# Performance work log

Measured on AMD Instinct MI355X. Metric: run time of the kernel, lower is better.

## Reference

```python
import jax, jax.numpy as jnp
import numpy as np

B, S, D, H = 2, 2048, 1024, 16
DH = D // H
DFF = 4 * D
EPS = 1e-5


def layernorm(x, g, b):
    mu = jnp.mean(x, axis=-1, keepdims=True)
    var = jnp.mean(jnp.square(x - mu), axis=-1, keepdims=True)
    return (x - mu) * jax.lax.rsqrt(var + EPS) * g + b


def setup_inputs() -> dict:
    key = jax.random.key(0)
    ks = jax.random.split(key, 12)
    s = 0.02
    return {
        "x": jax.random.normal(ks[0], (B, S, D), dtype=jnp.float32),
        "ln1_g": jnp.ones((D,), jnp.float32),
        "ln1_b": jnp.zeros((D,), jnp.float32),
        "Wq": jax.random.normal(ks[1], (D, D), jnp.float32) * s,
        "bq": jnp.zeros((D,), jnp.float32),
        "Wk": jax.random.normal(ks[2], (D, D), jnp.float32) * s,
        "bk": jnp.zeros((D,), jnp.float32),
        "Wv": jax.random.normal(ks[3], (D, D), jnp.float32) * s,
        "bv": jnp.zeros((D,), jnp.float32),
        "Wo": jax.random.normal(ks[4], (D, D), jnp.float32) * s,
        "bo": jnp.zeros((D,), jnp.float32),
        "ln2_g": jnp.ones((D,), jnp.float32),
        "ln2_b": jnp.zeros((D,), jnp.float32),
        "W1": jax.random.normal(ks[5], (D, DFF), jnp.float32) * s,
        "b1": jnp.zeros((DFF,), jnp.float32),
        "W2": jax.random.normal(ks[6], (DFF, D), jnp.float32) * s,
        "b2": jnp.zeros((D,), jnp.float32),
    }


def block(x, ln1_g, ln1_b, Wq, bq, Wk, bk, Wv, bv, Wo, bo, ln2_g, ln2_b, W1, b1, W2, b2):
    h = layernorm(x, ln1_g, ln1_b)
    # projections -> [B, H, S, DH]
    q = (h @ Wq + bq).reshape(B, S, H, DH).transpose(0, 2, 1, 3)
    k = (h @ Wk + bk).reshape(B, S, H, DH).transpose(0, 2, 1, 3)
    v = (h @ Wv + bv).reshape(B, S, H, DH).transpose(0, 2, 1, 3)
    scores = jnp.einsum('bhqd,bhkd->bhqk', q, k) / jnp.sqrt(jnp.float32(DH))
    causal = jnp.tril(jnp.ones((S, S), dtype=bool))  # True = keep
    scores = jnp.where(causal, scores, -jnp.inf)
    attn = jax.nn.softmax(scores, axis=-1)
    out = jnp.einsum('bhqk,bhkd->bhqd', attn, v)
    out = out.transpose(0, 2, 1, 3).reshape(B, S, D)
    x = x + out @ Wo + bo
    h2 = layernorm(x, ln2_g, ln2_b)
    ff = jax.nn.gelu(h2 @ W1 + b1, approximate=False) @ W2 + b2
    return x + ff


def reference(x, ln1_g, ln1_b, Wq, bq, Wk, bk, Wv, bv, Wo, bo, ln2_g, ln2_b, W1, b1, W2, b2):
    return block(x, ln1_g, ln1_b, Wq, bq, Wk, bk, Wv, bv, Wo, bo, ln2_g, ln2_b, W1, b1, W2, b2)
```

## Files before the change

### kernel.cpp

```cpp
#include <hip/hip_runtime.h>
#include <cstdint>
#include <cstddef>


#define DEV static __device__ __forceinline__

typedef unsigned short u16;
typedef __bf16 bf16x8 __attribute__((ext_vector_type(8)));
typedef u16    u16x8  __attribute__((ext_vector_type(8)));
typedef u16    u16x4  __attribute__((ext_vector_type(4)));
typedef float  f32x4  __attribute__((ext_vector_type(4)));

#define AEXP2(x) __builtin_amdgcn_exp2f(x)

DEV u16 f2bf(float f) {
  unsigned u = __builtin_bit_cast(unsigned, f);
  u += 0x7fffu + ((u >> 16) & 1u);
  return (u16)(u >> 16);
}

DEV void gl16(const void* g, void* l) {
  __builtin_amdgcn_global_load_lds(
      (const __attribute__((address_space(1))) unsigned*)g,
      (__attribute__((address_space(3))) unsigned*)l, 16, 0, 0);
}

__global__ __launch_bounds__(256)
void tconv(const float* __restrict__ in, u16* __restrict__ out, int R, int C)
{
  __shared__ float tile[32][33];
  const int tx = threadIdx.x & 31, ty = threadIdx.x >> 5;
  const int r0 = blockIdx.y * 32, c0 = blockIdx.x * 32;
#pragma unroll
  for (int i = 0; i < 4; ++i)
    tile[ty + 8*i][tx] = in[(size_t)(r0 + ty + 8*i) * C + c0 + tx];
  __syncthreads();
#pragma unroll
  for (int i = 0; i < 4; ++i)
    out[(size_t)(c0 + ty + 8*i) * R + r0 + tx] = f2bf(tile[tx][ty + 8*i]);
}

__global__ __launch_bounds__(256)
void tconv4(const float* __restrict__ w0, const float* __restrict__ w1,
            const float* __restrict__ w2, const float* __restrict__ w3,
            u16* __restrict__ q0, u16* __restrict__ q1,
            u16* __restrict__ q2, u16* __restrict__ q3)
{
  __shared__ float tile[32][33];
  const int z = blockIdx.z;
  const float* in = z == 0 ? w0 : z == 1 ? w1 : z == 2 ? w2 : w3;
  u16* out       = z == 0 ? q0 : z == 1 ? q1 : z == 2 ? q2 : q3;
  const int tx = threadIdx.x & 31, ty = threadIdx.x >> 5;
  const int r0 = blockIdx.y * 32, c0 = blockIdx.x * 32;
#pragma unroll
  for (int i = 0; i < 4; ++i)
    tile[ty + 8*i][tx] = in[(size_t)(r0 + ty + 8*i) * 1024 + c0 + tx];
  __syncthreads();
#pragma unroll
  for (int i = 0; i < 4; ++i)
    out[(size_t)(c0 + ty + 8*i) * 1024 + r0 + tx] = f2bf(tile[tx][ty + 8*i]);
}

__global__ __launch_bounds__(256)
void ln_fwd(const float* __restrict__ x, const float* __restrict__ g,
            const float* __restrict__ b, u16* __restrict__ out)
{
  const int row = blockIdx.x, t = threadIdx.x;
  const float4 v = ((const float4*)(x + (size_t)row * 1024))[t];
  float s1 = v.x + v.y + v.z + v.w;
  float s2 = v.x*v.x + v.y*v.y + v.z*v.z + v.w*v.w;
#pragma unroll
  for (int d = 1; d < 64; d <<= 1) {
    s1 += __shfl_xor(s1, d, 64);
    s2 += __shfl_xor(s2, d, 64);
  }
  __shared__ float sh[8];
  const int w = t >> 6;
  if ((t & 63) == 0) { sh[w] = s1; sh[w + 4] = s2; }
  __syncthreads();
  s1 = sh[0] + sh[1] + sh[2] + sh[3];
  s2 = sh[4] + sh[5] + sh[6] + sh[7];
  const float mu  = s1 * (1.0f / 1024.0f);
  const float var = s2 * (1.0f / 1024.0f) - mu * mu;
  const float rs  = rsqrtf(var + 1e-5f);
  const float4 gv = ((const float4*)g)[t];
  const float4 bv = ((const float4*)b)[t];
  u16x4 o;
  o[0] = f2bf((v.x - mu) * rs * gv.x + bv.x);
  o[1] = f2bf((v.y - mu) * rs * gv.y + bv.y);
  o[2] = f2bf((v.z - mu) * rs * gv.z + bv.z);
  o[3] = f2bf((v.w - mu) * rs * gv.w + bv.w);
  *(u16x4*)(out + (size_t)row * 1024 + t * 4) = o;
}

#define EPI_QKV  0
#define EPI_RES  1
#define EPI_GELU 2

#define QSCALE 0.180421f

template<int EPI, int BM, bool DBUF, int CM>
__global__ __launch_bounds__(256)
void gemm_bt(const u16* __restrict__ A, const u16* __restrict__ Bt,
             const float* __restrict__ b0, const float* __restrict__ b1,
             const float* __restrict__ b2, const float* __restrict__ res,
             float* __restrict__ outf, u16* __restrict__ o0,
             u16* __restrict__ o1, u16* __restrict__ o2,
             int N, int K)
{
  constexpr int MI = BM / 32;
  constexpr int RA = BM / 32;
  constexpr int NB = DBUF ? 2 : 1;
  __shared__ u16 As[NB][BM * 64];
  __shared__ u16 Bs[NB][128 * 64];
  const int t = threadIdx.x, lane = t & 63, w = t >> 6;
  const int wr = w >> 1, wc = w & 1;
  const int d = blockIdx.x + gridDim.x * blockIdx.y;
  const int rr = d >> 3;
  const int m0 = ((d & 7) * CM + rr % CM) * BM;
  const int n0 = (rr / CM) * 128;
  const int li = lane & 15, lg = lane >> 4;

  const int srow = t >> 3;
  const int schunk = (t & 7) ^ (srow & 7);
  const u16* Ag = A  + (size_t)(m0 + srow) * K + schunk * 8;
  const u16* Bg = Bt + (size_t)(n0 + srow) * K + schunk * 8;

  auto STG = [&](int k0, int b) {
#pragma unroll
    for (int p = 0; p < RA; ++p)
      gl16(Ag + k0 + (size_t)(p * 32) * K, &As[b][t * 8 + p * 2048]);
#pragma unroll
    for (int p = 0; p < 4; ++p)
      gl16(Bg + k0 + (size_t)(p * 32) * K, &Bs[b][t * 8 + p * 2048]);
  };

  f32x4 acc[MI][4] = {};

  if (DBUF) { STG(0, 0); __syncthreads(); }

  for (int k0 = 0; k0 < K; k0 += 64) {
    int cur;
    if (DBUF) {
      cur = (k0 >> 6) & 1;
      if (k0 + 64 < K) STG(k0 + 64, 1 - cur);
    } else {
      cur = 0;
      __syncthreads();
      STG(k0, 0);
      __syncthreads();
    }
    const int swz = (li & 7) << 4;
#pragma unroll
    for (int ks = 0; ks < 2; ++ks) {
      bf16x8 af[MI], bfr[4];
#pragma unroll
      for (int i = 0; i < MI; ++i) {
        const int Ra = wr * (MI * 16) + i * 16 + li;
        af[i] = *(const bf16x8*)((const char*)As[cur] + Ra * 128 +
                                 ((ks * 64 + lg * 16) ^ swz));
      }
#pragma unroll
      for (int i = 0; i < 4; ++i) {
        const int Rb = wc * 64 + i * 16 + li;
        bfr[i] = *(const bf16x8*)((const char*)Bs[cur] + Rb * 128 +
                                  ((ks * 64 + lg * 16) ^ swz));
      }
#pragma unroll
      for (int mi = 0; mi < MI; ++mi)
#pragma unroll
        for (int ni = 0; ni < 4; ++ni)
          acc[mi][ni] = __builtin_amdgcn_mfma_f32_16x16x32_bf16(
              af[mi], bfr[ni], acc[mi][ni], 0, 0, 0);
    }
    if (DBUF) __syncthreads();
  }

  const int crow = wr * (MI * 16) + lg * 4;
  const int ccol = wc * 64 + li;

  if (EPI == EPI_QKV) {
    const int which = n0 >> 10;
    const float* bias = which == 0 ? b0 : which == 1 ? b1 : b2;
    const int nn0 = n0 & 1023;
    if (which == 2) {
#pragma unroll
      for (int mi = 0; mi < MI; ++mi)
#pragma unroll
        for (int ni = 0; ni < 4; ++ni) {
          const int gm0 = m0 + crow + mi * 16;
          const int b_ = gm0 >> 11, s_ = gm0 & 2047;
          const int gc = nn0 + ccol + ni * 16;
          const int h_ = gc >> 6, d_ = gc & 63;
          u16x4 pk;
#pragma unroll
          for (int r = 0; r < 4; ++r) pk[r] = f2bf(acc[mi][ni][r] + bias[gc]);
          *(u16x4*)(o2 + ((size_t)(b_ * 16 + h_) * 64 + d_) * 2048 + s_) = pk;
        }
    } else {
      u16* outp = which == 0 ? o0 : o1;
      const float sc = which == 0 ? QSCALE : 1.0f;
#pragma unroll
      for (int mi = 0; mi < MI; ++mi)
#pragma unroll
        for (int ni = 0; ni < 4; ++ni)
#pragma unroll
          for (int r = 0; r < 4; ++r) {
            const int gm = m0 + crow + mi * 16 + r;
            const int gc = nn0 + ccol + ni * 16;
            const float v = (acc[mi][ni][r] + bias[gc]) * sc;
            const int b_ = gm >> 11, s_ = gm & 2047;
            const int h_ = gc >> 6,  d_ = gc & 63;
            outp[((size_t)(b_ * 16 + h_) * 2048 + s_) * 64 + d_] = f2bf(v);
          }
    }
  } else {
#pragma unroll
    for (int mi = 0; mi < MI; ++mi)
#pragma unroll
      for (int ni = 0; ni < 4; ++ni)
#pragma unroll
        for (int r = 0; r < 4; ++r) {
          const int gm = m0 + crow + mi * 16 + r;
          const int gn = n0 + ccol + ni * 16;
          const float v = acc[mi][ni][r] + b0[gn];
          if (EPI == EPI_RES) {
            const size_t o = (size_t)gm * N + gn;
            outf[o] = v + res[o];
          } else {
            const float y = 0.7978845608f * (v + 0.044715f * v * v * v);
            const float e = AEXP2(fminf(y * 2.8853900818f, 80.0f));
            const float gl = v * e * __builtin_amdgcn_rcpf(e + 1.0f);
            o0[(size_t)gm * N + gn] = f2bf(gl);
          }
        }
  }
}

__global__ __launch_bounds__(512, 4)
void attn_fwd(const u16* __restrict__ qb, const u16* __restrict__ kb,
              const u16* __restrict__ vtb, u16* __restrict__ ob)
{
  __shared__ u16 Ks[2][128 * 64];
  __shared__ u16 Vt[2][64 * 128];
  __shared__ u16 Ps[8][16 * 64];
  const int t = threadIdx.x, w = t >> 6, lane = t & 63;
  const int li = lane & 15, lg = lane >> 4;
  const int bh = blockIdx.y;
  const int bx = blockIdx.x;
  const int qt = (bh & 16) ? (15 - bx) : bx;
  const int q0 = qt * 128;

  const size_t qrow = (size_t)bh * 2048 + q0 + w * 16 + li;
  const bf16x8 aq0 = *(const bf16x8*)(qb + qrow * 64 + lg * 8);
  const bf16x8 aq1 = *(const bf16x8*)(qb + qrow * 64 + lg * 8 + 32);

  f32x4 o[4] = {};
  float mrun[4], lrun[4];
#pragma unroll
  for (int r = 0; r < 4; ++r) { mrun[r] = -1e30f; lrun[r] = 0.0f; }

  const u16* kbase = kb  + (size_t)bh * 2048 * 64;
  const u16* vbase = vtb + (size_t)bh * 64 * 2048;
  const int ntile = qt + 1;

  const int kchunk = (t & 7)  ^ ((t >> 3) & 7);
  const int vchunk = (t & 15) ^ ((t >> 4) & 15);
  const u16* kg = kbase + (size_t)(t >> 3) * 64 + kchunk * 8;
  const u16* vg = vbase + (size_t)(t >> 4) * 2048 + vchunk * 8;

#define STAGE(tk_, b_)                                              \
  {                                                                 \
    const int kv0s = (tk_) * 128;                                   \
    gl16(kg + (size_t)kv0s * 64,        &Ks[b_][t * 8]);            \
    gl16(kg + (size_t)(kv0s + 64) * 64, &Ks[b_][t * 8 + 4096]);     \
    gl16(vg + kv0s,                     &Vt[b_][t * 8]);            \
    gl16(vg + kv0s + (size_t)32 * 2048, &Vt[b_][t * 8 + 4096]);     \
  }

  STAGE(0, 0);
  __syncthreads();

  for (int tk = 0; tk < ntile; ++tk) {
    const int cur = tk & 1;
    const int kv0 = tk * 128;
    if (tk + 1 < ntile) STAGE(tk + 1, 1 - cur);

    f32x4 s[8];
    __builtin_amdgcn_s_setprio(1);
#pragma unroll
    for (int cf = 0; cf < 8; ++cf) {
      const int row = cf * 16 + li;
      const char* kc = (const char*)Ks[cur] + row * 128;
      const int sw = (row & 7) << 4;
      const bf16x8 bk0 = *(const bf16x8*)(kc + ((lg * 16)      ^ sw));
      const bf16x8 bk1 = *(const bf16x8*)(kc + ((lg * 16 + 64) ^ sw));
      f32x4 z = {};
      z = __builtin_amdgcn_mfma_f32_16x16x32_bf16(aq0, bk0, z, 0, 0, 0);
      z = __builtin_amdgcn_mfma_f32_16x16x32_bf16(aq1, bk1, z, 0, 0, 0);
      s[cf] = z;
    }
    __builtin_amdgcn_s_setprio(0);
    const int row0 = q0 + w * 16 + lg * 4;
    if (tk == ntile - 1) {
#pragma unroll
      for (int cf = 0; cf < 8; ++cf)
#pragma unroll
        for (int r = 0; r < 4; ++r)
          if (kv0 + cf * 16 + li > row0 + r) s[cf][r] = -1e30f;
    }

    float pmax[4];
#pragma unroll
    for (int r = 0; r < 4; ++r) {
      float mx = s[0][r];
#pragma unroll
      for (int cf = 1; cf < 8; ++cf) mx = fmaxf(mx, s[cf][r]);
      pmax[r] = mx;
    }
#pragma unroll
    for (int d = 1; d < 16; d <<= 1)
#pragma unroll
      for (int r = 0; r < 4; ++r)
        pmax[r] = fmaxf(pmax[r], __shfl_xor(pmax[r], d, 64));

    bool need = false;
#pragma unroll
    for (int r = 0; r < 4; ++r) need = need || (pmax[r] > mrun[r] + 11.5f);
    if (__any((int)need)) {
#pragma unroll
      for (int r = 0; r < 4; ++r) {
        const float mnew = fmaxf(mrun[r], pmax[r]);
        const float scl  = AEXP2(mrun[r] - mnew);
        lrun[r] *= scl;
#pragma unroll
        for (int n = 0; n < 4; ++n) o[n][r] *= scl;
        mrun[r] = mnew;
      }
    }
    float ps[4] = {0.f, 0.f, 0.f, 0.f};
#pragma unroll
    for (int cf = 0; cf < 8; ++cf)
#pragma unroll
      for (int r = 0; r < 4; ++r) {
        const float pv = AEXP2(s[cf][r] - mrun[r]);
        s[cf][r] = pv;
        ps[r] += pv;
      }
#pragma unroll
    for (int d = 1; d < 16; d <<= 1)
#pragma unroll
      for (int r = 0; r < 4; ++r)
        ps[r] += __shfl_xor(ps[r], d, 64);
#pragma unroll
    for (int r = 0; r < 4; ++r) lrun[r] += ps[r];

#pragma unroll
    for (int kh = 0; kh < 2; ++kh) {
#pragma unroll
      for (int cf2 = 0; cf2 < 4; ++cf2)
#pragma unroll
        for (int r = 0; r < 4; ++r) {
          const int prow = lg * 4 + r;
          const int pcolB = (cf2 * 16 + li) * 2;
          *(u16*)((char*)Ps[w] + prow * 128 + (pcolB ^ ((prow & 7) << 4))) =
              f2bf(s[kh * 4 + cf2][r]);
        }
      __builtin_amdgcn_s_setprio(1);
#pragma unroll
      for (int ks = 0; ks < 2; ++ks) {
        const char* pc = (const char*)Ps[w] + li * 128;
        const bf16x8 ap =
            *(const bf16x8*)(pc + ((lg * 16 + ks * 64) ^ ((li & 7) << 4)));
#pragma unroll
        for (int n = 0; n < 4; ++n) {
          const int vrow = n * 16 + li;
          const char* vc = (const char*)Vt[cur] + vrow * 256;
          const int colB = lg * 16 + ks * 64 + kh * 128;
          const bf16x8 bv =
              *(const bf16x8*)(vc + (colB ^ ((vrow & 15) << 4)));
          o[n] = __builtin_amdgcn_mfma_f32_16x16x32_bf16(ap, bv, o[n], 0, 0, 0);
        }
      }
      __builtin_amdgcn_s_setprio(0);
    }

    __syncthreads();
  }
#undef STAGE

  float inv[4];
#pragma unroll
  for (int r = 0; r < 4; ++r) inv[r] = __builtin_amdgcn_rcpf(lrun[r]);
  const int b_ = bh >> 4, h_ = bh & 15;
#pragma unroll
  for (int n = 0; n < 4; ++n)
#pragma unroll
    for (int r = 0; r < 4; ++r) {
      const int rowg = q0 + w * 16 + lg * 4 + r;
      ob[((size_t)b_ * 2048 + rowg) * 1024 + h_ * 64 + n * 16 + li] =
          f2bf(o[n][r] * inv[r]);
    }
}

extern "C" void kernel_launch(void* const* d_in, const int* in_sizes, int n_in,
                              void* d_out, int out_size, void* d_ws, size_t ws_size,
                              hipStream_t stream) {
  const float* x    = (const float*)d_in[0];
  const float* ln1g = (const float*)d_in[1];
  const float* ln1b = (const float*)d_in[2];
  const float* Wq   = (const float*)d_in[3];
  const float* bq   = (const float*)d_in[4];
  const float* Wk   = (const float*)d_in[5];
  const float* bk   = (const float*)d_in[6];
  const float* Wv   = (const float*)d_in[7];
  const float* bv   = (const float*)d_in[8];
  const float* Wo   = (const float*)d_in[9];
  const float* bo   = (const float*)d_in[10];
  const float* ln2g = (const float*)d_in[11];
  const float* ln2b = (const float*)d_in[12];
  const float* W1   = (const float*)d_in[13];
  const float* b1   = (const float*)d_in[14];
  const float* W2   = (const float*)d_in[15];
  const float* b2   = (const float*)d_in[16];

  char* ws = (char*)d_ws;
  const size_t MB = 1u << 20;
  u16*   hb   = (u16*)(ws + 0);
  u16*   Wqt  = (u16*)(ws + 8  * MB);
  u16*   Wkt  = (u16*)(ws + 10 * MB);
  u16*   Wvt  = (u16*)(ws + 12 * MB);
  u16*   Wot  = (u16*)(ws + 14 * MB);
  u16*   W1t  = (u16*)(ws + 16 * MB);
  u16*   W2t  = (u16*)(ws + 24 * MB);
  u16*   qbuf = (u16*)(ws + 32 * MB);
  u16*   kbuf = (u16*)(ws + 40 * MB);
  u16*   aob  = (u16*)(ws + 48 * MB);
  u16*   vtb  = (u16*)(ws + 56 * MB);
  float* x2   = (float*)(ws + 64 * MB);
  u16*   h2   = hb;
  u16*   ff1  = qbuf;

  const dim3 blk(256);
  tconv4<<<dim3(32, 32, 4), blk, 0, stream>>>(Wq, Wk, Wv, Wo, Wqt, Wkt, Wvt, Wot);
  tconv<<<dim3(128, 32), blk, 0, stream>>>(W1, W1t, 1024, 4096);
  tconv<<<dim3(32, 128), blk, 0, stream>>>(W2, W2t, 4096, 1024);

  ln_fwd<<<4096, blk, 0, stream>>>(x, ln1g, ln1b, hb);

  gemm_bt<EPI_QKV, 128, false, 4><<<dim3(24, 32), blk, 0, stream>>>(
      hb, Wqt, bq, bk, bv, nullptr, nullptr, qbuf, kbuf, vtb, 3072, 1024);

  attn_fwd<<<dim3(16, 32), dim3(512), 0, stream>>>(qbuf, kbuf, vtb, aob);

  gemm_bt<EPI_RES, 64, true, 8><<<dim3(8, 64), blk, 0, stream>>>(
      aob, Wot, bo, nullptr, nullptr, x, x2, nullptr, nullptr, nullptr, 1024, 1024);

  ln_fwd<<<4096, blk, 0, stream>>>(x2, ln2g, ln2b, h2);

  gemm_bt<EPI_GELU, 128, false, 4><<<dim3(32, 32), blk, 0, stream>>>(
      h2, W1t, b1, nullptr, nullptr, nullptr, nullptr, ff1, nullptr, nullptr, 4096, 1024);

  gemm_bt<EPI_RES, 64, true, 8><<<dim3(8, 64), blk, 0, stream>>>(
      ff1, W2t, b2, nullptr, nullptr, x2, (float*)d_out, nullptr, nullptr, nullptr, 1024, 4096);
}
```

Before: 241.1 us.

## Replace double buffering with three-stage LDS pipeline using explicit vmcnt waits

The pipelined GEMM path now uses three LDS buffers, prefetching two k-steps ahead. It waits with a partial s_waitcnt vmcnt so the next stage's global-to-LDS loads can stay in flight, and uses a single barrier per step instead of two. This aims to hide global load latency behind MFMA work. It costs more shared memory, which may lower occupancy, and the hard-coded vmcnt literal is only valid for BM=64.

```diff
diff --git a/kernel.cpp b/kernel.cpp
--- a/kernel.cpp
+++ b/kernel.cpp
@@ -99,7 +99,7 @@
 
 #define QSCALE 0.180421f
 
-template<int EPI, int BM, bool DBUF, int CM>
+template<int EPI, int BM, bool PIPE, int CM>
 __global__ __launch_bounds__(256)
 void gemm_bt(const u16* __restrict__ A, const u16* __restrict__ Bt,
              const float* __restrict__ b0, const float* __restrict__ b1,
@@ -110,7 +110,8 @@
 {
   constexpr int MI = BM / 32;
   constexpr int RA = BM / 32;
-  constexpr int NB = DBUF ? 2 : 1;
+  constexpr int NB = PIPE ? 3 : 1;
+  static_assert(!PIPE || BM == 64, "vmcnt literal assumes 6 loads/step");
   __shared__ u16 As[NB][BM * 64];
   __shared__ u16 Bs[NB][128 * 64];
   const int t = threadIdx.x, lane = t & 63, w = t >> 6;
@@ -136,21 +137,9 @@
   };
 
   f32x4 acc[MI][4] = {};
-
-  if (DBUF) { STG(0, 0); __syncthreads(); }
-
-  for (int k0 = 0; k0 < K; k0 += 64) {
-    int cur;
-    if (DBUF) {
-      cur = (k0 >> 6) & 1;
-      if (k0 + 64 < K) STG(k0 + 64, 1 - cur);
-    } else {
-      cur = 0;
-      __syncthreads();
-      STG(k0, 0);
-      __syncthreads();
-    }
-    const int swz = (li & 7) << 4;
+  const int swz = (li & 7) << 4;
+
+  auto COMPUTE = [&](int cur) {
 #pragma unroll
     for (int ks = 0; ks < 2; ++ks) {
       bf16x8 af[MI], bfr[4];
@@ -173,7 +162,33 @@
           acc[mi][ni] = __builtin_amdgcn_mfma_f32_16x16x32_bf16(
               af[mi], bfr[ni], acc[mi][ni], 0, 0, 0);
     }
-    if (DBUF) __syncthreads();
+  };
+
+  if (PIPE) {
+    STG(0, 0);
+    if (64 < K) STG(64, 1);
+    int cur = 0;
+    for (int k0 = 0; k0 < K; k0 += 64) {
+      if (k0 + 64 < K)
+        asm volatile("s_waitcnt vmcnt(6)" ::: "memory");
+      else
+        asm volatile("s_waitcnt vmcnt(0)" ::: "memory");
+      __builtin_amdgcn_s_barrier();
+      __builtin_amdgcn_sched_barrier(0);
+      COMPUTE(cur);
+      if (k0 + 128 < K) {
+        int nxt = cur + 2; if (nxt >= 3) nxt -= 3;
+        STG(k0 + 128, nxt);
+      }
+      cur = (cur + 1 == 3) ? 0 : cur + 1;
+    }
+  } else {
+    for (int k0 = 0; k0 < K; k0 += 64) {
+      __syncthreads();
+      STG(k0, 0);
+      __syncthreads();
+      COMPUTE(0);
+    }
   }
 
   const int crow = wr * (MI * 16) + lg * 4;
```

New measurement: 230.1 us. 1.05x faster.
